# Kernel tuning notes

Hardware: AMD Instinct MI355X
Metric: run time of the kernel (lower is better)

The kernel has to match this reference:

```python
import jax, jax.numpy as jnp
import numpy as np

B, T, L, H = 8, 32, 512, 768  # batch docs, decode steps, encoder length, BART-base hidden


def setup_inputs() -> dict:
    key = jax.random.key(0)
    ks = jax.random.split(key, 7)
    sc = 1.0 / np.sqrt(H).astype(np.float32)
    return {
        "encoder_hn": jax.random.normal(ks[0], (B, L, H), jnp.float32),
        "dec": jax.random.normal(ks[1], (B, T, H), jnp.float32),   # decoder_rnn outputs per step
        "W1": jax.random.normal(ks[2], (H, H), jnp.float32) * sc,  # nnW1 (no bias)
        "W2": jax.random.normal(ks[3], (H, H), jnp.float32) * sc,  # nnW2 (no bias)
        "v": jax.random.normal(ks[4], (H,), jnp.float32) * sc,     # nnV (no bias)
        "starts": jax.random.randint(ks[5], (B, T), 0, 128, jnp.int32),  # ragged slice start per step
        "lens": jax.random.randint(ks[6], (B,), 300, L + 1, jnp.int32),  # curL per document
    }


def reference(encoder_hn, dec, W1, W2, v, starts, lens):
    # pointerLayer batched over (b, t):
    #   WE = nnW1(en)          -> [B, L, H]
    #   WD = nnW2(di expanded) -> [B, T, H]
    #   scores = selu( nnV( selu(WE + WD) ) )  over positions [start, len)
    WE = jnp.einsum('blh,kh->blk', encoder_hn, W1)                 # [B, L, H]
    WD = jnp.einsum('bth,kh->btk', dec, W2)                        # [B, T, H]
    act = jax.nn.selu(WE[:, None, :, :] + WD[:, :, None, :])      # [B, T, L, H]
    scores = jax.nn.selu(jnp.einsum('btlh,h->btl', act, v))       # [B, T, L]
    # ragged slice curencoder_hn[start:curL] expressed as a mask
    pos = jnp.arange(L, dtype=jnp.int32)
    mask = (pos[None, None, :] >= starts[:, :, None]) & \
           (pos[None, None, :] < lens[:, None, None])              # [B, T, L]
    NEG = jnp.asarray(-1e30, scores.dtype)
    logp = jax.nn.log_softmax(jnp.where(mask, scores, NEG), axis=-1)
    return jnp.where(mask, logp, jnp.zeros((), logp.dtype))       # masked log-probs [B, T, L]
```

## Files before the change

### kernel.cpp

```cpp
#include <hip/hip_runtime.h>
#include <math.h>

constexpr int Bn = 8, Tn = 32, Ln = 512, Hn = 768;

typedef __attribute__((ext_vector_type(8))) short bf16x8;
typedef __attribute__((ext_vector_type(4))) float f32x4;

__device__ __forceinline__ short f2bf(float x) {
    unsigned u = __float_as_uint(x);
    u += 0x7FFFu + ((u >> 16) & 1u);
    return (short)(u >> 16);
}
__device__ __forceinline__ float bf2f(unsigned short s) {
    return __uint_as_float(((unsigned)s) << 16);
}

constexpr float kScale = 1.0507009873554804934193349852946f;
constexpr float kAS    = 1.7580993408473768f;

__device__ __forceinline__ float selu(float x) {
    return x > 0.f ? kScale * x : fmaf(kAS, __expf(x), -kAS);
}

__global__ __launch_bounds__(256) void cvt_bf16_multi(
    const float* __restrict__ s0, short* __restrict__ d0, int c0,
    const float* __restrict__ s1, short* __restrict__ d1, int c1,
    const float* __restrict__ s2, short* __restrict__ d2, int c2,
    const float* __restrict__ s3, short* __restrict__ d3, int c3)
{
    const int i = blockIdx.x * 256 + threadIdx.x;
    if (i >= c3) return;
    const float* s; short* d; int off;
    if (i < c0)      { s = s0; d = d0; off = i; }
    else if (i < c1) { s = s1; d = d1; off = i - c0; }
    else if (i < c2) { s = s2; d = d2; off = i - c1; }
    else             { s = s3; d = d3; off = i - c2; }
    const float4 f = ((const float4*)s)[off];
    short4 r;
    r.x = f2bf(f.x); r.y = f2bf(f.y); r.z = f2bf(f.z); r.w = f2bf(f.w);
    ((short4*)d)[off] = r;
}

__global__ __launch_bounds__(256) void gemm_bf16_nt(
    const short* __restrict__ A,
    const short* __restrict__ Bm,
    unsigned short* __restrict__ C,
    int M, int N, int K)
{
    constexpr int BM = 128, BN = 64, BK = 32;
    __shared__ __align__(16) short As[BM * BK];
    __shared__ __align__(16) short Bs[BN * BK];

    const int tid  = threadIdx.x;
    const int lane = tid & 63;
    const int wv   = tid >> 6;
    const int quad = lane >> 4;
    const int l16  = lane & 15;
    const int wm   = (wv & 1) * 64;
    const int wn   = (wv >> 1) * 32;
    const int bm   = blockIdx.x * BM;
    const int bn   = blockIdx.y * BN;

    const int sr = lane >> 2;
    const int kq = (lane & 3) << 3;

    f32x4 acc[4][2] = {};

    for (int k0 = 0; k0 < K; k0 += BK) {
        {
            const int ra = wv * 16 + sr;
            __builtin_amdgcn_global_load_lds(
                (const __attribute__((address_space(1))) unsigned int*)(A + (size_t)(bm + ra) * K + k0 + kq),
                (__attribute__((address_space(3))) unsigned int*)(As + ra * BK + kq),
                16, 0, 0);
            __builtin_amdgcn_global_load_lds(
                (const __attribute__((address_space(1))) unsigned int*)(A + (size_t)(bm + 64 + ra) * K + k0 + kq),
                (__attribute__((address_space(3))) unsigned int*)(As + (64 + ra) * BK + kq),
                16, 0, 0);
            __builtin_amdgcn_global_load_lds(
                (const __attribute__((address_space(1))) unsigned int*)(Bm + (size_t)(bn + ra) * K + k0 + kq),
                (__attribute__((address_space(3))) unsigned int*)(Bs + ra * BK + kq),
                16, 0, 0);
        }
        __syncthreads();

        bf16x8 af[4], bfr[2];
#pragma unroll
        for (int i = 0; i < 4; ++i)
            af[i] = *(const bf16x8*)&As[(wm + i * 16 + l16) * BK + quad * 8];
#pragma unroll
        for (int j = 0; j < 2; ++j)
            bfr[j] = *(const bf16x8*)&Bs[(wn + j * 16 + l16) * BK + quad * 8];
#pragma unroll
        for (int i = 0; i < 4; ++i)
#pragma unroll
            for (int j = 0; j < 2; ++j)
                acc[i][j] = __builtin_amdgcn_mfma_f32_16x16x32_bf16(af[i], bfr[j], acc[i][j], 0, 0, 0);
        __syncthreads();
    }

#pragma unroll
    for (int i = 0; i < 4; ++i)
#pragma unroll
        for (int j = 0; j < 2; ++j)
#pragma unroll
            for (int rr = 0; rr < 4; ++rr) {
                const int row = bm + wm + i * 16 + quad * 4 + rr;
                const int col = bn + wn + j * 16 + l16;
                C[(size_t)row * N + col] = (unsigned short)f2bf(acc[i][j][rr]);
            }
}

__global__ __launch_bounds__(256) void scores_kernel(
    const unsigned short* __restrict__ WE,
    const unsigned short* __restrict__ WD,
    const float* __restrict__ v,
    float* __restrict__ sc)
{
    const int bid = blockIdx.x;
    const int b = bid & 7;
    const int r = bid >> 3;
    const int t = r & 31;
    const int chunk = r >> 5;
    const int bt = b * Tn + t;
    const int lane = threadIdx.x & 63;
    const int wv = threadIdx.x >> 6;
    const int l0 = chunk * 64 + wv * 16;

    float wdr[12], vr[12];
#pragma unroll
    for (int j = 0; j < 3; ++j) {
        const int h = (lane << 2) + (j << 8);
        const ushort4 wdu = *(const ushort4*)(WD + (size_t)bt * Hn + h);
        const float4 vv = *(const float4*)(v + h);
        wdr[j * 4 + 0] = bf2f(wdu.x); wdr[j * 4 + 1] = bf2f(wdu.y);
        wdr[j * 4 + 2] = bf2f(wdu.z); wdr[j * 4 + 3] = bf2f(wdu.w);
        vr[j * 4 + 0] = vv.x; vr[j * 4 + 1] = vv.y;
        vr[j * 4 + 2] = vv.z; vr[j * 4 + 3] = vv.w;
    }

    const unsigned short* WEb = WE + (size_t)b * Ln * Hn;

    for (int i = 0; i < 16; ++i) {
        const int l = l0 + i;
        const unsigned short* row = WEb + (size_t)l * Hn;
        float s = 0.f;
#pragma unroll
        for (int j = 0; j < 3; ++j) {
            const int h = (lane << 2) + (j << 8);
            const ushort4 weu = *(const ushort4*)(row + h);
            float x;
            x = bf2f(weu.x) + wdr[j * 4 + 0]; s = fmaf(selu(x), vr[j * 4 + 0], s);
            x = bf2f(weu.y) + wdr[j * 4 + 1]; s = fmaf(selu(x), vr[j * 4 + 1], s);
            x = bf2f(weu.z) + wdr[j * 4 + 2]; s = fmaf(selu(x), vr[j * 4 + 2], s);
            x = bf2f(weu.w) + wdr[j * 4 + 3]; s = fmaf(selu(x), vr[j * 4 + 3], s);
        }
#pragma unroll
        for (int off = 32; off > 0; off >>= 1)
            s += __shfl_xor(s, off, 64);
        if (lane == 0)
            sc[(size_t)bt * Ln + l] = selu(s);
    }
}

__global__ __launch_bounds__(512) void softmax_kernel(
    const float* __restrict__ sc,
    const int* __restrict__ starts,
    const int* __restrict__ lens,
    float* __restrict__ out)
{
    __shared__ float red[16];
    const int bt = blockIdx.x;
    const int b = bt / Tn;
    const int tid = threadIdx.x;
    const int lane = tid & 63;
    const int wv = tid >> 6;

    const int start = starts[bt];
    const int len = lens[b];
    const int l = tid;
    const bool msk = (l >= start) && (l < len);
    const float val = sc[(size_t)bt * Ln + l];

    float mx = msk ? val : -1e30f;
#pragma unroll
    for (int off = 32; off > 0; off >>= 1)
        mx = fmaxf(mx, __shfl_xor(mx, off, 64));
    if (lane == 0) red[wv] = mx;
    __syncthreads();
    mx = red[0];
#pragma unroll
    for (int i = 1; i < 8; ++i) mx = fmaxf(mx, red[i]);

    float sm = msk ? __expf(val - mx) : 0.f;
#pragma unroll
    for (int off = 32; off > 0; off >>= 1)
        sm += __shfl_xor(sm, off, 64);
    if (lane == 0) red[8 + wv] = sm;
    __syncthreads();
    float tot = red[8];
#pragma unroll
    for (int i = 1; i < 8; ++i) tot += red[8 + i];

    const float logZ = mx + __logf(tot);
    out[(size_t)bt * Ln + l] = msk ? (val - logZ) : 0.f;
}

extern "C" void kernel_launch(void* const* d_in, const int* in_sizes, int n_in,
                              void* d_out, int out_size, void* d_ws, size_t ws_size,
                              hipStream_t stream) {
    const float* enc    = (const float*)d_in[0];
    const float* dec    = (const float*)d_in[1];
    const float* W1     = (const float*)d_in[2];
    const float* W2     = (const float*)d_in[3];
    const float* v      = (const float*)d_in[4];
    const int*   starts = (const int*)d_in[5];
    const int*   lens   = (const int*)d_in[6];
    float* out = (float*)d_out;

    constexpr int n_enc = Bn * Ln * Hn;
    constexpr int n_dec = Bn * Tn * Hn;
    constexpr int n_w   = Hn * Hn;
    constexpr int n_sc  = Bn * Tn * Ln;

    const size_t need = (size_t)(n_enc + n_dec + 2 * n_w) * 2
                      + (size_t)(n_enc + n_dec) * 2
                      + (size_t)n_sc * 4;
    if (ws_size < need) return;

    short* enc16 = (short*)d_ws;
    short* dec16 = enc16 + n_enc;
    short* w1_16 = dec16 + n_dec;
    short* w2_16 = w1_16 + n_w;
    unsigned short* WE16 = (unsigned short*)(w2_16 + n_w);
    unsigned short* WD16 = WE16 + n_enc;
    float* sc = (float*)(WD16 + n_dec);

    constexpr int c0 = n_enc / 4;
    constexpr int c1 = c0 + n_dec / 4;
    constexpr int c2 = c1 + n_w / 4;
    constexpr int c3 = c2 + n_w / 4;
    cvt_bf16_multi<<<dim3((c3 + 255) / 256), dim3(256), 0, stream>>>(
        enc, enc16, c0, dec, dec16, c1, W1, w1_16, c2, W2, w2_16, c3);

    gemm_bf16_nt<<<dim3((Bn * Ln) / 128, Hn / 64), dim3(256), 0, stream>>>(
        enc16, w1_16, WE16, Bn * Ln, Hn, Hn);
    gemm_bf16_nt<<<dim3((Bn * Tn) / 128, Hn / 64), dim3(256), 0, stream>>>(
        dec16, w2_16, WD16, Bn * Tn, Hn, Hn);

    scores_kernel<<<dim3(2048), dim3(256), 0, stream>>>(WE16, WD16, v, sc);
    softmax_kernel<<<dim3(Bn * Tn), dim3(512), 0, stream>>>(sc, starts, lens, out);
}
```

Before: 139.6 us.

## Merge both projection GEMMs into one launch, widen tile, batch score rows

The two bf16 GEMMs (encoder·W1 and decoder·W2) now run in a single launch that picks its operand set by block index. The N tile grows from 64 to 128, so each wave computes a 64x64 output patch. The scores kernel loads four WE rows at once and interleaves their selu-dot accumulation and wave reductions. This targets launch overhead and aims to raise memory-level parallelism and operand reuse. The cost is fewer GEMM blocks (grid halves in N) and higher register pressure in both kernels.

```diff
diff --git a/kernel.cpp b/kernel.cpp
--- a/kernel.cpp
+++ b/kernel.cpp
@@ -41,15 +41,23 @@
     ((short4*)d)[off] = r;
 }
 
-__global__ __launch_bounds__(256) void gemm_bf16_nt(
-    const short* __restrict__ A,
-    const short* __restrict__ Bm,
-    unsigned short* __restrict__ C,
-    int M, int N, int K)
-{
-    constexpr int BM = 128, BN = 64, BK = 32;
+__global__ __launch_bounds__(256) void gemm2_bf16_nt(
+    const short* __restrict__ A1, const short* __restrict__ B1,
+    unsigned short* __restrict__ C1, int M1,
+    const short* __restrict__ A2, const short* __restrict__ B2,
+    unsigned short* __restrict__ C2,
+    int N, int K)
+{
+    constexpr int BM = 128, BN = 128, BK = 32;
     __shared__ __align__(16) short As[BM * BK];
     __shared__ __align__(16) short Bs[BN * BK];
+
+    const int nblk1 = M1 / BM;
+    const int bx = blockIdx.x;
+    const short* A; const short* Bm; unsigned short* C; int bm;
+    if (bx < nblk1) { A = A1; Bm = B1; C = C1; bm = bx * BM; }
+    else            { A = A2; Bm = B2; C = C2; bm = (bx - nblk1) * BM; }
+    const int bn = blockIdx.y * BN;
 
     const int tid  = threadIdx.x;
     const int lane = tid & 63;
@@ -57,44 +65,40 @@
     const int quad = lane >> 4;
     const int l16  = lane & 15;
     const int wm   = (wv & 1) * 64;
-    const int wn   = (wv >> 1) * 32;
-    const int bm   = blockIdx.x * BM;
-    const int bn   = blockIdx.y * BN;
+    const int wn   = (wv >> 1) * 64;
 
     const int sr = lane >> 2;
     const int kq = (lane & 3) << 3;
 
-    f32x4 acc[4][2] = {};
+    f32x4 acc[4][4] = {};
 
     for (int k0 = 0; k0 < K; k0 += BK) {
-        {
-            const int ra = wv * 16 + sr;
-            __builtin_amdgcn_global_load_lds(
-                (const __attribute__((address_space(1))) unsigned int*)(A + (size_t)(bm + ra) * K + k0 + kq),
-                (__attribute__((address_space(3))) unsigned int*)(As + ra * BK + kq),
-                16, 0, 0);
-            __builtin_amdgcn_global_load_lds(
-                (const __attribute__((address_space(1))) unsigned int*)(A + (size_t)(bm + 64 + ra) * K + k0 + kq),
-                (__attribute__((address_space(3))) unsigned int*)(As + (64 + ra) * BK + kq),
-                16, 0, 0);
-            __builtin_amdgcn_global_load_lds(
-                (const __attribute__((address_space(1))) unsigned int*)(Bm + (size_t)(bn + ra) * K + k0 + kq),
-                (__attribute__((address_space(3))) unsigned int*)(Bs + ra * BK + kq),
-                16, 0, 0);
-        }
+        const int ra = wv * 16 + sr;
+        __builtin_amdgcn_global_load_lds(
+            (const __attribute__((address_space(1))) unsigned int*)(A + (size_t)(bm + ra) * K + k0 + kq),
+            (__attribute__((address_space(3))) unsigned int*)(As + ra * BK + kq), 16, 0, 0);
+        __builtin_amdgcn_global_load_lds(
+            (const __attribute__((address_space(1))) unsigned int*)(A + (size_t)(bm + 64 + ra) * K + k0 + kq),
+            (__attribute__((address_space(3))) unsigned int*)(As + (64 + ra) * BK + kq), 16, 0, 0);
+        __builtin_amdgcn_global_load_lds(
+            (const __attribute__((address_space(1))) unsigned int*)(Bm + (size_t)(bn + ra) * K + k0 + kq),
+            (__attribute__((address_space(3))) unsigned int*)(Bs + ra * BK + kq), 16, 0, 0);
+        __builtin_amdgcn_global_load_lds(
+            (const __attribute__((address_space(1))) unsigned int*)(Bm + (size_t)(bn + 64 + ra) * K + k0 + kq),
+            (__attribute__((address_space(3))) unsigned int*)(Bs + (64 + ra) * BK + kq), 16, 0, 0);
         __syncthreads();
 
-        bf16x8 af[4], bfr[2];
+        bf16x8 af[4], bfr[4];
 #pragma unroll
         for (int i = 0; i < 4; ++i)
             af[i] = *(const bf16x8*)&As[(wm + i * 16 + l16) * BK + quad * 8];
 #pragma unroll
-        for (int j = 0; j < 2; ++j)
+        for (int j = 0; j < 4; ++j)
             bfr[j] = *(const bf16x8*)&Bs[(wn + j * 16 + l16) * BK + quad * 8];
 #pragma unroll
         for (int i = 0; i < 4; ++i)
 #pragma unroll
-            for (int j = 0; j < 2; ++j)
+            for (int j = 0; j < 4; ++j)
                 acc[i][j] = __builtin_amdgcn_mfma_f32_16x16x32_bf16(af[i], bfr[j], acc[i][j], 0, 0, 0);
         __syncthreads();
     }
@@ -102,7 +106,7 @@
 #pragma unroll
     for (int i = 0; i < 4; ++i)
 #pragma unroll
-        for (int j = 0; j < 2; ++j)
+        for (int j = 0; j < 4; ++j)
 #pragma unroll
             for (int rr = 0; rr < 4; ++rr) {
                 const int row = bm + wm + i * 16 + quad * 4 + rr;
@@ -141,25 +145,40 @@
 
     const unsigned short* WEb = WE + (size_t)b * Ln * Hn;
 
-    for (int i = 0; i < 16; ++i) {
-        const int l = l0 + i;
-        const unsigned short* row = WEb + (size_t)l * Hn;
-        float s = 0.f;
+#pragma unroll
+    for (int g = 0; g < 4; ++g) {
+        const int lg = l0 + g * 4;
+        ushort4 weu[4][3];
+#pragma unroll
+        for (int rr = 0; rr < 4; ++rr) {
+            const unsigned short* row = WEb + (size_t)(lg + rr) * Hn;
+#pragma unroll
+            for (int j = 0; j < 3; ++j)
+                weu[rr][j] = *(const ushort4*)(row + (lane << 2) + (j << 8));
+        }
+        float s[4] = {0.f, 0.f, 0.f, 0.f};
 #pragma unroll
         for (int j = 0; j < 3; ++j) {
-            const int h = (lane << 2) + (j << 8);
-            const ushort4 weu = *(const ushort4*)(row + h);
-            float x;
-            x = bf2f(weu.x) + wdr[j * 4 + 0]; s = fmaf(selu(x), vr[j * 4 + 0], s);
-            x = bf2f(weu.y) + wdr[j * 4 + 1]; s = fmaf(selu(x), vr[j * 4 + 1], s);
-            x = bf2f(weu.z) + wdr[j * 4 + 2]; s = fmaf(selu(x), vr[j * 4 + 2], s);
-            x = bf2f(weu.w) + wdr[j * 4 + 3]; s = fmaf(selu(x), vr[j * 4 + 3], s);
-        }
-#pragma unroll
-        for (int off = 32; off > 0; off >>= 1)
-            s += __shfl_xor(s, off, 64);
-        if (lane == 0)
-            sc[(size_t)bt * Ln + l] = selu(s);
+#pragma unroll
+            for (int rr = 0; rr < 4; ++rr) {
+                float x;
+                x = bf2f(weu[rr][j].x) + wdr[j * 4 + 0]; s[rr] = fmaf(selu(x), vr[j * 4 + 0], s[rr]);
+                x = bf2f(weu[rr][j].y) + wdr[j * 4 + 1]; s[rr] = fmaf(selu(x), vr[j * 4 + 1], s[rr]);
+                x = bf2f(weu[rr][j].z) + wdr[j * 4 + 2]; s[rr] = fmaf(selu(x), vr[j * 4 + 2], s[rr]);
+                x = bf2f(weu[rr][j].w) + wdr[j * 4 + 3]; s[rr] = fmaf(selu(x), vr[j * 4 + 3], s[rr]);
+            }
+        }
+#pragma unroll
+        for (int off = 32; off > 0; off >>= 1) {
+#pragma unroll
+            for (int rr = 0; rr < 4; ++rr)
+                s[rr] += __shfl_xor(s[rr], off, 64);
+        }
+        if (lane == 0) {
+#pragma unroll
+            for (int rr = 0; rr < 4; ++rr)
+                sc[(size_t)bt * Ln + lg + rr] = selu(s[rr]);
+        }
     }
 }
 
@@ -243,10 +262,10 @@
     cvt_bf16_multi<<<dim3((c3 + 255) / 256), dim3(256), 0, stream>>>(
         enc, enc16, c0, dec, dec16, c1, W1, w1_16, c2, W2, w2_16, c3);
 
-    gemm_bf16_nt<<<dim3((Bn * Ln) / 128, Hn / 64), dim3(256), 0, stream>>>(
-        enc16, w1_16, WE16, Bn * Ln, Hn, Hn);
-    gemm_bf16_nt<<<dim3((Bn * Tn) / 128, Hn / 64), dim3(256), 0, stream>>>(
-        dec16, w2_16, WD16, Bn * Tn, Hn, Hn);
+    gemm2_bf16_nt<<<dim3((Bn * Ln) / 128 + (Bn * Tn) / 128, Hn / 128),
+                    dim3(256), 0, stream>>>(
+        enc16, w1_16, WE16, Bn * Ln,
+        dec16, w2_16, WD16, Hn, Hn);
 
     scores_kernel<<<dim3(2048), dim3(256), 0, stream>>>(WE16, WD16, v, sc);
     softmax_kernel<<<dim3(Bn * Tn), dim3(512), 0, stream>>>(sc, starts, lens, out);
```

Result: faster. 130.4 us (-6.6%).
